# Performance work log

Hardware: AMD Instinct MI355X
Metric: run time of the kernel (lower is better)

The kernel has to match this reference:

```python
import jax, jax.numpy as jnp
import numpy as np

N_QUBITS = 4
N_LAYERS = 2
BATCH = 524288


def _apply_1q(state, U, axis):
    # state: [B, 2,2,2,2]; U: [2,2] (shared) or [B,2,2] (per-sample); axis = wire index + 1
    s = jnp.moveaxis(state, axis, -1)
    if U.ndim == 3:
        s = jnp.einsum('bij,b...j->b...i', U, s)
    else:
        s = jnp.einsum('ij,...j->...i', U, s)
    return jnp.moveaxis(s, -1, axis)


def _apply_cz(state, a, b):
    # diagonal CZ: flip sign where both qubits are |1>
    sign = jnp.array([[1.0, 1.0], [1.0, -1.0]], dtype=state.dtype)
    shape = [1] * state.ndim
    shape[a] = 2
    shape[b] = 2
    return state * sign.reshape(shape)


def _quantum_expval(feats, w):
    # feats: [B, n_qubits] angles; w: [n_layers, n_qubits, 3] Rot params
    B = feats.shape[0]
    state = jnp.zeros((B,) + (2,) * N_QUBITS, jnp.complex64)
    state = state.at[(slice(None),) + (0,) * N_QUBITS].set(1.0)
    # per-sample RY embedding
    for i in range(N_QUBITS):
        c = jnp.cos(feats[:, i] * 0.5)
        s = jnp.sin(feats[:, i] * 0.5)
        U = jnp.stack([jnp.stack([c, -s], -1), jnp.stack([s, c], -1)], -2).astype(jnp.complex64)
        state = _apply_1q(state, U, i + 1)
    # variational layers: Rot(phi,theta,omega) = RZ(omega) RY(theta) RZ(phi), then CZ chain
    for l in range(N_LAYERS):
        for i in range(N_QUBITS):
            phi, theta, omega = w[l, i, 0], w[l, i, 1], w[l, i, 2]
            ct = jnp.cos(theta * 0.5)
            st = jnp.sin(theta * 0.5)
            U = jnp.stack([
                jnp.stack([jnp.exp(-0.5j * (phi + omega)) * ct, -jnp.exp(0.5j * (phi - omega)) * st]),
                jnp.stack([jnp.exp(-0.5j * (phi - omega)) * st, jnp.exp(0.5j * (phi + omega)) * ct]),
            ]).astype(jnp.complex64)
            state = _apply_1q(state, U, i + 1)
        for i in range(N_QUBITS - 1):
            state = _apply_cz(state, i + 1, i + 2)
    probs = jnp.square(jnp.abs(state))
    p = probs.sum(axis=tuple(range(2, N_QUBITS + 1)))  # marginal of wire 0 -> [B, 2]
    return (p[:, 0] - p[:, 1]).astype(jnp.float32)  # <Z_0>


def setup_inputs() -> dict:
    key = jax.random.key(0)
    ks = jax.random.split(key, 12)
    f = jnp.float32
    return {
        'text': jax.random.normal(ks[0], (BATCH, 16), f),
        'image': jax.random.normal(ks[1], (BATCH, 48), f),
        'tW1': jax.random.normal(ks[2], (16, 32), f) * 0.25,
        'tb1': jnp.zeros((32,), f),
        'tW2': jax.random.normal(ks[3], (32, N_QUBITS), f) * 0.18,
        'tb2': jnp.zeros((N_QUBITS,), f),
        'iW1': jax.random.normal(ks[4], (48, 64), f) * 0.14,
        'ib1': jnp.zeros((64,), f),
        'iW2': jax.random.normal(ks[5], (64, N_QUBITS), f) * 0.125,
        'ib2': jnp.zeros((N_QUBITS,), f),
        'qweights': jax.random.normal(ks[6], (N_LAYERS, N_QUBITS, 3), f),
        'cW1': jax.random.normal(ks[7], (1, 16), f),
        'cb1': jnp.zeros((16,), f),
        'cW2': jax.random.normal(ks[8], (16, 2), f) * 0.25,
        'cb2': jnp.zeros((2,), f),
    }


def reference(text, image, tW1, tb1, tW2, tb2, iW1, ib1, iW2, ib2, qweights, cW1, cb1, cW2, cb2):
    tf = jax.nn.relu(text @ tW1 + tb1) @ tW2 + tb2      # [B, 4]
    imf = jax.nn.relu(image @ iW1 + ib1) @ iW2 + ib2    # [B, 4]
    feats = (tf + imf) * 0.5                             # [B, 4]
    q = _quantum_expval(feats, qweights)                 # [B]
    h = jax.nn.relu(q[:, None] @ cW1 + cb1)              # [B, 16]
    return h @ cW2 + cb2                                 # [B, 2]
```

## Files before the change

kernel.cpp:

```cpp
#include <hip/hip_runtime.h>
#include <math.h>

#define NQ 4
#define NL 2

typedef __attribute__((ext_vector_type(8))) short short8v;
typedef __attribute__((ext_vector_type(4))) float f32x4;

__device__ inline unsigned short f2bf(float x){
    unsigned u = __float_as_uint(x);
    u += 0x7FFFu + ((u >> 16) & 1u);
    return (unsigned short)(u >> 16);
}
__device__ inline float bf2f(unsigned short h){
    return __uint_as_float(((unsigned)h) << 16);
}
__device__ inline void split8(const float* x, short8v& hi, short8v& lo){
    #pragma unroll
    for (int e = 0; e < 8; ++e){
        unsigned short h = f2bf(x[e]);
        hi[e] = (short)h;
        lo[e] = (short)f2bf(x[e] - bf2f(h));
    }
}
#define PK(i, val) { unsigned short h_ = f2bf(val); hi[i] = (short)h_; lo[i] = (short)f2bf((val) - bf2f(h_)); }
__device__ inline void pack8(float4 a, float4 b, short8v& hi, short8v& lo){
    PK(0, a.x) PK(1, a.y) PK(2, a.z) PK(3, a.w)
    PK(4, b.x) PK(5, b.y) PK(6, b.z) PK(7, b.w)
}
#undef PK

__global__ void qnn_precompute_A(const float* __restrict__ qw, float* __restrict__ A)
{
    __shared__ float Mre[16][16];
    __shared__ float Mim[16][16];
    int t = threadIdx.x;
    if (t < 16) {
        int j = t;
        float re[16], im[16];
        for (int b = 0; b < 16; ++b) { re[b] = (b == j) ? 1.f : 0.f; im[b] = 0.f; }
        for (int l = 0; l < NL; ++l) {
            for (int i = 0; i < NQ; ++i) {
                float phi   = qw[(l*NQ + i)*3 + 0];
                float theta = qw[(l*NQ + i)*3 + 1];
                float omega = qw[(l*NQ + i)*3 + 2];
                float ct, st; sincosf(0.5f*theta, &st, &ct);
                float ap = 0.5f*(phi + omega);
                float am = 0.5f*(phi - omega);
                float cap, sap, cam, sam;
                sincosf(ap, &sap, &cap);
                sincosf(am, &sam, &cam);
                float u00r =  cap*ct, u00i = -sap*ct;
                float u01r = -cam*st, u01i = -sam*st;
                float u10r =  cam*st, u10i = -sam*st;
                float u11r =  cap*ct, u11i =  sap*ct;
                int mask = 1 << (3 - i);
                for (int b = 0; b < 16; ++b) {
                    if (b & mask) continue;
                    int b1 = b | mask;
                    float a0r = re[b],  a0i = im[b];
                    float a1r = re[b1], a1i = im[b1];
                    re[b]  = u00r*a0r - u00i*a0i + u01r*a1r - u01i*a1i;
                    im[b]  = u00r*a0i + u00i*a0r + u01r*a1i + u01i*a1r;
                    re[b1] = u10r*a0r - u10i*a0i + u11r*a1r - u11i*a1i;
                    im[b1] = u10r*a0i + u10i*a0r + u11r*a1i + u11i*a1r;
                }
            }
            for (int b = 0; b < 16; ++b) {
                float sgn = 1.f;
                if ((b & 0xC) == 0xC) sgn = -sgn;
                if ((b & 0x6) == 0x6) sgn = -sgn;
                if ((b & 0x3) == 0x3) sgn = -sgn;
                re[b] *= sgn; im[b] *= sgn;
            }
        }
        for (int b = 0; b < 16; ++b) { Mre[j][b] = re[b]; Mim[j][b] = im[b]; }
    }
    __syncthreads();
    {
        int j = t >> 4, k = t & 15;
        float s = 0.f;
        #pragma unroll
        for (int b = 0; b < 16; ++b) {
            float sg = (b & 8) ? -1.f : 1.f;
            s += sg * (Mre[j][b]*Mre[k][b] + Mim[j][b]*Mim[k][b]);
        }
        A[j*16 + k] = s;
    }
}

__device__ inline void po_update(float (&po)[4][4], const f32x4& cc, const float4& w2){
    #pragma unroll
    for (int r = 0; r < 4; ++r){
        float h = fmaxf(cc[r], 0.f);
        po[r][0] = fmaf(h, w2.x, po[r][0]);
        po[r][1] = fmaf(h, w2.y, po[r][1]);
        po[r][2] = fmaf(h, w2.z, po[r][2]);
        po[r][3] = fmaf(h, w2.w, po[r][3]);
    }
}
__device__ inline void reduce_po(float (&po)[4][4]){
    #pragma unroll
    for (int r = 0; r < 4; ++r)
        #pragma unroll
        for (int o = 0; o < 4; ++o){
            float v = po[r][o];
            v += __shfl_xor(v, 1);
            v += __shfl_xor(v, 2);
            v += __shfl_xor(v, 4);
            v += __shfl_xor(v, 8);
            po[r][o] = v;
        }
}
__device__ inline float4 pick_row(const float (&po)[4][4], int c){
    float4 v;
    if      (c == 0) v = make_float4(po[0][0], po[0][1], po[0][2], po[0][3]);
    else if (c == 1) v = make_float4(po[1][0], po[1][1], po[1][2], po[1][3]);
    else if (c == 2) v = make_float4(po[2][0], po[2][1], po[2][2], po[2][3]);
    else             v = make_float4(po[3][0], po[3][1], po[3][2], po[3][3]);
    return v;
}

#define STEP3(ACC, BH, BL, AH, AL)                                          \
    ACC = __builtin_amdgcn_mfma_f32_16x16x32_bf16(AH, BH, ACC, 0, 0, 0);    \
    ACC = __builtin_amdgcn_mfma_f32_16x16x32_bf16(AH, BL, ACC, 0, 0, 0);    \
    ACC = __builtin_amdgcn_mfma_f32_16x16x32_bf16(AL, BH, ACC, 0, 0, 0);

__global__ __launch_bounds__(256, 4) void qnn_main(
    const float* __restrict__ text, const float* __restrict__ image,
    const float* __restrict__ tW1, const float* __restrict__ tb1,
    const float* __restrict__ tW2, const float* __restrict__ tb2,
    const float* __restrict__ iW1, const float* __restrict__ ib1,
    const float* __restrict__ iW2, const float* __restrict__ ib2,
    const float* __restrict__ A,
    const float* __restrict__ cW1, const float* __restrict__ cb1,
    const float* __restrict__ cW2, const float* __restrict__ cb2,
    float* __restrict__ out, int B)
{
    __shared__ short8v WimgH[4][2][64];
    __shared__ short8v WimgL[4][2][64];
    __shared__ short8v WtxtH[2][64];
    __shared__ short8v WtxtL[2][64];
    __shared__ float4  feats[256];

    const int t    = threadIdx.x;
    const int lane = t & 63;
    const int wv   = t >> 6;
    const int g    = lane >> 4;
    const int c    = lane & 15;
    const long long blockBase = (long long)blockIdx.x * 256;

    #pragma unroll
    for (int s = t; s < 512; s += 256){
        int nt = s >> 7, ks = (s >> 6) & 1, ln = s & 63;
        int gg = ln >> 4, cc_ = ln & 15;
        float x[8];
        #pragma unroll
        for (int e = 0; e < 8; ++e){
            int k = ks*32 + 8*gg + e;
            x[e] = (k < 48) ? iW1[k*64 + nt*16 + cc_] : 0.f;
        }
        short8v h, l; split8(x, h, l);
        WimgH[nt][ks][ln] = h;
        WimgL[nt][ks][ln] = l;
    }
    if (t < 128){
        int nt = t >> 6, ln = t & 63;
        int gg = ln >> 4, cc_ = ln & 15;
        float x[8];
        #pragma unroll
        for (int e = 0; e < 8; ++e){
            int k = 8*gg + e;
            x[e] = (k < 16) ? tW1[k*32 + nt*16 + cc_] : 0.f;
        }
        short8v h, l; split8(x, h, l);
        WtxtH[nt][ln] = h;
        WtxtL[nt][ln] = l;
    }
    __syncthreads();

    const float bI0 = ib1[c],      bI1 = ib1[16 + c];
    const float bI2 = ib1[32 + c], bI3 = ib1[48 + c];
    const float bT0 = tb1[c],      bT1 = tb1[16 + c];

    #pragma unroll 1
    for (int ms = 0; ms < 4; ++ms){
        long long m = blockBase + wv*64 + ms*16 + c;
        if (m >= B) m = B - 1;
        const float* irow = image + m*48;
        const float* trow = text  + m*16;

        const float4 z = make_float4(0.f, 0.f, 0.f, 0.f);
        float4 i0a = *(const float4*)(irow + 8*g);
        float4 i0b = *(const float4*)(irow + 8*g + 4);
        float4 i1a = z, i1b = z, t0a = z, t0b = z;
        if (g < 2){
            i1a = *(const float4*)(irow + 32 + 8*g);
            i1b = *(const float4*)(irow + 36 + 8*g);
            t0a = *(const float4*)(trow + 8*g);
            t0b = *(const float4*)(trow + 8*g + 4);
        }

        f32x4 a0 = { bI0, bI0, bI0, bI0 };
        f32x4 a1 = { bI1, bI1, bI1, bI1 };
        f32x4 a2 = { bI2, bI2, bI2, bI2 };
        f32x4 a3 = { bI3, bI3, bI3, bI3 };
        f32x4 a4 = { bT0, bT0, bT0, bT0 };
        f32x4 a5 = { bT1, bT1, bT1, bT1 };

        short8v Ah, Al;

        pack8(i0a, i0b, Ah, Al);
        { short8v bh = WimgH[0][0][lane], bl = WimgL[0][0][lane]; STEP3(a0, bh, bl, Ah, Al) }
        { short8v bh = WimgH[1][0][lane], bl = WimgL[1][0][lane]; STEP3(a1, bh, bl, Ah, Al) }
        { short8v bh = WimgH[2][0][lane], bl = WimgL[2][0][lane]; STEP3(a2, bh, bl, Ah, Al) }
        { short8v bh = WimgH[3][0][lane], bl = WimgL[3][0][lane]; STEP3(a3, bh, bl, Ah, Al) }
        __builtin_amdgcn_sched_barrier(0);

        pack8(i1a, i1b, Ah, Al);
        { short8v bh = WimgH[0][1][lane], bl = WimgL[0][1][lane]; STEP3(a0, bh, bl, Ah, Al) }
        { short8v bh = WimgH[1][1][lane], bl = WimgL[1][1][lane]; STEP3(a1, bh, bl, Ah, Al) }
        { short8v bh = WimgH[2][1][lane], bl = WimgL[2][1][lane]; STEP3(a2, bh, bl, Ah, Al) }
        { short8v bh = WimgH[3][1][lane], bl = WimgL[3][1][lane]; STEP3(a3, bh, bl, Ah, Al) }
        __builtin_amdgcn_sched_barrier(0);

        pack8(t0a, t0b, Ah, Al);
        { short8v bh = WtxtH[0][lane], bl = WtxtL[0][lane]; STEP3(a4, bh, bl, Ah, Al) }
        { short8v bh = WtxtH[1][lane], bl = WtxtL[1][lane]; STEP3(a5, bh, bl, Ah, Al) }
        __builtin_amdgcn_sched_barrier(0);

        float po[4][4];
        #pragma unroll
        for (int r = 0; r < 4; ++r)
            #pragma unroll
            for (int o = 0; o < 4; ++o) po[r][o] = 0.f;

        { float4 w2 = *(const float4*)(iW2 + (c)*4);      po_update(po, a0, w2); }
        { float4 w2 = *(const float4*)(iW2 + (16+c)*4);   po_update(po, a1, w2); }
        { float4 w2 = *(const float4*)(iW2 + (32+c)*4);   po_update(po, a2, w2); }
        { float4 w2 = *(const float4*)(iW2 + (48+c)*4);   po_update(po, a3, w2); }
        { float4 w2 = *(const float4*)(tW2 + (c)*4);      po_update(po, a4, w2); }
        { float4 w2 = *(const float4*)(tW2 + (16+c)*4);   po_update(po, a5, w2); }

        reduce_po(po);
        if (c < 4)
            feats[wv*64 + ms*16 + 4*g + c] = pick_row(po, c);
        __builtin_amdgcn_sched_barrier(0);
    }

    __syncthreads();

    long long samp = blockBase + t;
    if (samp < B){
        float4 f4 = feats[t];
        float acc[4];
        acc[0] = tb2[0] + ib2[0] + f4.x;
        acc[1] = tb2[1] + ib2[1] + f4.y;
        acc[2] = tb2[2] + ib2[2] + f4.z;
        acc[3] = tb2[3] + ib2[3] + f4.w;

        float cth[4], sth[4];
        #pragma unroll
        for (int i = 0; i < 4; ++i){
            float f = acc[i] * 0.25f;
            __sincosf(f, &sth[i], &cth[i]);
        }
        float p01[4] = { cth[0]*cth[1], cth[0]*sth[1], sth[0]*cth[1], sth[0]*sth[1] };
        float p23[4] = { cth[2]*cth[3], cth[2]*sth[3], sth[2]*cth[3], sth[2]*sth[3] };
        float psi[16];
        #pragma unroll
        for (int x = 0; x < 4; ++x)
            #pragma unroll
            for (int y = 0; y < 4; ++y)
                psi[x*4+y] = p01[x] * p23[y];

        float q = 0.f;
        #pragma unroll
        for (int j = 0; j < 16; ++j){
            float row = 0.f;
            #pragma unroll
            for (int k = 0; k < 16; ++k) row = fmaf(A[j*16+k], psi[k], row);
            q = fmaf(psi[j], row, q);
        }

        float o0 = cb2[0], o1 = cb2[1];
        #pragma unroll
        for (int j = 0; j < 16; ++j){
            float h = fmaxf(fmaf(q, cW1[j], cb1[j]), 0.f);
            o0 = fmaf(h, cW2[j*2+0], o0);
            o1 = fmaf(h, cW2[j*2+1], o1);
        }
        float2* o2 = (float2*)out;
        o2[samp] = make_float2(o0, o1);
    }
}

extern "C" void kernel_launch(void* const* d_in, const int* in_sizes, int n_in,
                              void* d_out, int out_size, void* d_ws, size_t ws_size,
                              hipStream_t stream)
{
    const float* text  = (const float*)d_in[0];
    const float* image = (const float*)d_in[1];
    const float* tW1   = (const float*)d_in[2];
    const float* tb1   = (const float*)d_in[3];
    const float* tW2   = (const float*)d_in[4];
    const float* tb2   = (const float*)d_in[5];
    const float* iW1   = (const float*)d_in[6];
    const float* ib1   = (const float*)d_in[7];
    const float* iW2   = (const float*)d_in[8];
    const float* ib2   = (const float*)d_in[9];
    const float* qw    = (const float*)d_in[10];
    const float* cW1   = (const float*)d_in[11];
    const float* cb1   = (const float*)d_in[12];
    const float* cW2   = (const float*)d_in[13];
    const float* cb2   = (const float*)d_in[14];

    float* A = (float*)d_ws;
    int B = in_sizes[0] / 16;

    qnn_precompute_A<<<1, 256, 0, stream>>>(qw, A);

    int block = 256;
    int grid = (B + block - 1) / block;
    qnn_main<<<grid, block, 0, stream>>>(
        text, image, tW1, tb1, tW2, tb2, iW1, ib1, iW2, ib2,
        A, cW1, cb1, cW2, cb2, (float*)d_out, B);
}
```

Before: 246.1 us.

## Split fused kernel into feature-MLP kernel and quantum-tail kernel via workspace

Breaks the single fused kernel into two launches. The first computes the MFMA-based MLP features and writes them to a workspace buffer. The second reads those features and evaluates the quantum expectation and the classifier head at one sample per thread with higher occupancy. The aim is to stop the register- and occupancy-heavy tail from sharing a kernel with the MFMA stage. The cost is an extra launch and a round trip of 16 bytes per sample through global memory. The fused kernel is kept as a fallback when the workspace is too small.

```diff
diff --git a/kernel.cpp b/kernel.cpp
--- a/kernel.cpp
+++ b/kernel.cpp
@@ -99,6 +99,16 @@
         po[r][3] = fmaf(h, w2.w, po[r][3]);
     }
 }
+__device__ inline void po_updateB(float (&po)[4][4], const f32x4& cc, const float4& w2, float bb){
+    #pragma unroll
+    for (int r = 0; r < 4; ++r){
+        float h = fmaxf(cc[r] + bb, 0.f);
+        po[r][0] = fmaf(h, w2.x, po[r][0]);
+        po[r][1] = fmaf(h, w2.y, po[r][1]);
+        po[r][2] = fmaf(h, w2.z, po[r][2]);
+        po[r][3] = fmaf(h, w2.w, po[r][3]);
+    }
+}
 __device__ inline void reduce_po(float (&po)[4][4]){
     #pragma unroll
     for (int r = 0; r < 4; ++r)
@@ -126,7 +136,183 @@
     ACC = __builtin_amdgcn_mfma_f32_16x16x32_bf16(AH, BL, ACC, 0, 0, 0);    \
     ACC = __builtin_amdgcn_mfma_f32_16x16x32_bf16(AL, BH, ACC, 0, 0, 0);
 
-__global__ __launch_bounds__(256, 4) void qnn_main(
+__global__ __launch_bounds__(256, 4) void qnn_feats(
+    const float* __restrict__ text, const float* __restrict__ image,
+    const float* __restrict__ tW1, const float* __restrict__ tb1,
+    const float* __restrict__ tW2,
+    const float* __restrict__ iW1, const float* __restrict__ ib1,
+    const float* __restrict__ iW2,
+    float* __restrict__ featsOut, int B)
+{
+    __shared__ short8v WimgH[4][2][64];
+    __shared__ short8v WimgL[4][2][64];
+    __shared__ short8v WtxtH[2][64];
+    __shared__ short8v WtxtL[2][64];
+
+    const int t    = threadIdx.x;
+    const int lane = t & 63;
+    const int wv   = t >> 6;
+    const int g    = lane >> 4;
+    const int c    = lane & 15;
+    const long long blockBase = (long long)blockIdx.x * 256;
+
+    #pragma unroll
+    for (int s = t; s < 512; s += 256){
+        int nt = s >> 7, ks = (s >> 6) & 1, ln = s & 63;
+        int gg = ln >> 4, cc_ = ln & 15;
+        float x[8];
+        #pragma unroll
+        for (int e = 0; e < 8; ++e){
+            int k = ks*32 + 8*gg + e;
+            x[e] = (k < 48) ? iW1[k*64 + nt*16 + cc_] : 0.f;
+        }
+        short8v h, l; split8(x, h, l);
+        WimgH[nt][ks][ln] = h;
+        WimgL[nt][ks][ln] = l;
+    }
+    if (t < 128){
+        int nt = t >> 6, ln = t & 63;
+        int gg = ln >> 4, cc_ = ln & 15;
+        float x[8];
+        #pragma unroll
+        for (int e = 0; e < 8; ++e){
+            int k = 8*gg + e;
+            x[e] = (k < 16) ? tW1[k*32 + nt*16 + cc_] : 0.f;
+        }
+        short8v h, l; split8(x, h, l);
+        WtxtH[nt][ln] = h;
+        WtxtL[nt][ln] = l;
+    }
+    __syncthreads();
+
+    #pragma unroll 1
+    for (int ms = 0; ms < 4; ++ms){
+        long long m = blockBase + wv*64 + ms*16 + c;
+        if (m >= B) m = B - 1;
+        const float* irow = image + m*48;
+        const float* trow = text  + m*16;
+
+        const float4 z = make_float4(0.f, 0.f, 0.f, 0.f);
+        float4 i0a = *(const float4*)(irow + 8*g);
+        float4 i0b = *(const float4*)(irow + 8*g + 4);
+        float4 i1a = z, i1b = z, t0a = z, t0b = z;
+        if (g < 2){
+            i1a = *(const float4*)(irow + 32 + 8*g);
+            i1b = *(const float4*)(irow + 36 + 8*g);
+            t0a = *(const float4*)(trow + 8*g);
+            t0b = *(const float4*)(trow + 8*g + 4);
+        }
+
+        f32x4 a0 = { 0.f, 0.f, 0.f, 0.f };
+        f32x4 a1 = { 0.f, 0.f, 0.f, 0.f };
+        f32x4 a2 = { 0.f, 0.f, 0.f, 0.f };
+        f32x4 a3 = { 0.f, 0.f, 0.f, 0.f };
+        f32x4 a4 = { 0.f, 0.f, 0.f, 0.f };
+        f32x4 a5 = { 0.f, 0.f, 0.f, 0.f };
+
+        short8v Ah, Al;
+
+        pack8(i0a, i0b, Ah, Al);
+        { short8v bh = WimgH[0][0][lane], bl = WimgL[0][0][lane]; STEP3(a0, bh, bl, Ah, Al) }
+        { short8v bh = WimgH[1][0][lane], bl = WimgL[1][0][lane]; STEP3(a1, bh, bl, Ah, Al) }
+        { short8v bh = WimgH[2][0][lane], bl = WimgL[2][0][lane]; STEP3(a2, bh, bl, Ah, Al) }
+        { short8v bh = WimgH[3][0][lane], bl = WimgL[3][0][lane]; STEP3(a3, bh, bl, Ah, Al) }
+        __builtin_amdgcn_sched_barrier(0);
+
+        pack8(i1a, i1b, Ah, Al);
+        { short8v bh = WimgH[0][1][lane], bl = WimgL[0][1][lane]; STEP3(a0, bh, bl, Ah, Al) }
+        { short8v bh = WimgH[1][1][lane], bl = WimgL[1][1][lane]; STEP3(a1, bh, bl, Ah, Al) }
+        { short8v bh = WimgH[2][1][lane], bl = WimgL[2][1][lane]; STEP3(a2, bh, bl, Ah, Al) }
+        { short8v bh = WimgH[3][1][lane], bl = WimgL[3][1][lane]; STEP3(a3, bh, bl, Ah, Al) }
+        __builtin_amdgcn_sched_barrier(0);
+
+        pack8(t0a, t0b, Ah, Al);
+        { short8v bh = WtxtH[0][lane], bl = WtxtL[0][lane]; STEP3(a4, bh, bl, Ah, Al) }
+        { short8v bh = WtxtH[1][lane], bl = WtxtL[1][lane]; STEP3(a5, bh, bl, Ah, Al) }
+        __builtin_amdgcn_sched_barrier(0);
+
+        float po[4][4];
+        #pragma unroll
+        for (int r = 0; r < 4; ++r)
+            #pragma unroll
+            for (int o = 0; o < 4; ++o) po[r][o] = 0.f;
+
+        { float4 w2 = *(const float4*)(iW2 + (c)*4);      po_updateB(po, a0, w2, ib1[c]); }
+        { float4 w2 = *(const float4*)(iW2 + (16+c)*4);   po_updateB(po, a1, w2, ib1[16+c]); }
+        { float4 w2 = *(const float4*)(iW2 + (32+c)*4);   po_updateB(po, a2, w2, ib1[32+c]); }
+        { float4 w2 = *(const float4*)(iW2 + (48+c)*4);   po_updateB(po, a3, w2, ib1[48+c]); }
+        { float4 w2 = *(const float4*)(tW2 + (c)*4);      po_updateB(po, a4, w2, tb1[c]); }
+        { float4 w2 = *(const float4*)(tW2 + (16+c)*4);   po_updateB(po, a5, w2, tb1[16+c]); }
+
+        reduce_po(po);
+        if (c < 4){
+            long long sIdx = blockBase + wv*64 + ms*16 + 4*g + c;
+            if (sIdx < B)
+                ((float4*)featsOut)[sIdx] = pick_row(po, c);
+        }
+        __builtin_amdgcn_sched_barrier(0);
+    }
+}
+
+__global__ __launch_bounds__(256, 8) void qnn_tail(
+    const float* __restrict__ feats,
+    const float* __restrict__ tb2, const float* __restrict__ ib2,
+    const float* __restrict__ Aq,
+    const float* __restrict__ cW1, const float* __restrict__ cb1,
+    const float* __restrict__ cW2, const float* __restrict__ cb2,
+    float* __restrict__ out, int B)
+{
+    __shared__ float As[256];
+    const int t = threadIdx.x;
+    As[t] = Aq[t];
+    __syncthreads();
+
+    long long samp = (long long)blockIdx.x * 256 + t;
+    if (samp >= B) return;
+
+    float4 f4 = ((const float4*)feats)[samp];
+    float acc[4];
+    acc[0] = tb2[0] + ib2[0] + f4.x;
+    acc[1] = tb2[1] + ib2[1] + f4.y;
+    acc[2] = tb2[2] + ib2[2] + f4.z;
+    acc[3] = tb2[3] + ib2[3] + f4.w;
+
+    float cth[4], sth[4];
+    #pragma unroll
+    for (int i = 0; i < 4; ++i){
+        float f = acc[i] * 0.25f;
+        __sincosf(f, &sth[i], &cth[i]);
+    }
+    float p01[4] = { cth[0]*cth[1], cth[0]*sth[1], sth[0]*cth[1], sth[0]*sth[1] };
+    float p23[4] = { cth[2]*cth[3], cth[2]*sth[3], sth[2]*cth[3], sth[2]*sth[3] };
+    float psi[16];
+    #pragma unroll
+    for (int x = 0; x < 4; ++x)
+        #pragma unroll
+        for (int y = 0; y < 4; ++y)
+            psi[x*4+y] = p01[x] * p23[y];
+
+    float q = 0.f;
+    #pragma unroll
+    for (int j = 0; j < 16; ++j){
+        float row = 0.f;
+        #pragma unroll
+        for (int k = 0; k < 16; ++k) row = fmaf(As[j*16+k], psi[k], row);
+        q = fmaf(psi[j], row, q);
+    }
+
+    float o0 = cb2[0], o1 = cb2[1];
+    #pragma unroll
+    for (int j = 0; j < 16; ++j){
+        float h = fmaxf(fmaf(q, cW1[j], cb1[j]), 0.f);
+        o0 = fmaf(h, cW2[j*2+0], o0);
+        o1 = fmaf(h, cW2[j*2+1], o1);
+    }
+    float2* o2 = (float2*)out;
+    o2[samp] = make_float2(o0, o1);
+}
+
+__global__ __launch_bounds__(256, 4) void qnn_fused(
     const float* __restrict__ text, const float* __restrict__ image,
     const float* __restrict__ tW1, const float* __restrict__ tb1,
     const float* __restrict__ tW2, const float* __restrict__ tb2,
@@ -322,7 +508,17 @@
 
     int block = 256;
     int grid = (B + block - 1) / block;
-    qnn_main<<<grid, block, 0, stream>>>(
-        text, image, tW1, tb1, tW2, tb2, iW1, ib1, iW2, ib2,
-        A, cW1, cb1, cW2, cb2, (float*)d_out, B);
-}
+    size_t need = 1024 + (size_t)B * 16;
+
+    if (ws_size >= need){
+        float* featsWs = (float*)((char*)d_ws + 1024);
+        qnn_feats<<<grid, block, 0, stream>>>(
+            text, image, tW1, tb1, tW2, iW1, ib1, iW2, featsWs, B);
+        qnn_tail<<<grid, block, 0, stream>>>(
+            featsWs, tb2, ib2, A, cW1, cb1, cW2, cb2, (float*)d_out, B);
+    } else {
+        qnn_fused<<<grid, block, 0, stream>>>(
+            text, image, tW1, tb1, tW2, tb2, iW1, ib1, iW2, ib2,
+            A, cW1, cb1, cW2, cb2, (float*)d_out, B);
+    }
+}
```

After: 236.7 us. -3.8%, faster.
